# Optimization experiments

Measured on AMD Instinct MI355X. Metric: run time of the kernel, lower is better.

Reference implementation:

```python
import jax, jax.numpy as jnp
import numpy as np
import math

D_MODEL = 1024
NUM_HEADS = 16
HEAD_DIM = D_MODEL // NUM_HEADS


def _sinusoidal_pe(seq_len, dim, dtype=jnp.float32):
    # Matches RotaryPositionEmbedding buffer: pe[:,0::2]=sin, pe[:,1::2]=cos
    pos = jnp.arange(seq_len, dtype=jnp.float32)[:, None]            # [S,1]
    div = jnp.exp(jnp.arange(0, dim, 2, dtype=jnp.float32) * (-math.log(10000.0) / dim))  # [dim/2]
    ang = pos * div[None, :]                                          # [S,dim/2]
    pe = jnp.stack([jnp.sin(ang), jnp.cos(ang)], axis=-1).reshape(seq_len, dim)
    return pe.astype(dtype)


def setup_inputs() -> dict:
    key = jax.random.key(0)
    ks = jax.random.split(key, 11)
    B, S, D = 4, 1024, D_MODEL
    s = 1.0 / math.sqrt(D)
    inp = {
        "q": jax.random.normal(ks[0], (B, S, D), jnp.float32),
        "k": jax.random.normal(ks[1], (B, S, D), jnp.float32),
        "v": jax.random.normal(ks[2], (B, S, D), jnp.float32),
        "Wq": jax.random.normal(ks[3], (D, D), jnp.float32) * s,
        "bq": jax.random.normal(ks[4], (D,), jnp.float32) * s,
        "Wk": jax.random.normal(ks[5], (D, D), jnp.float32) * s,
        "bk": jax.random.normal(ks[6], (D,), jnp.float32) * s,
        "Wv": jax.random.normal(ks[7], (D, D), jnp.float32) * s,
        "bv": jax.random.normal(ks[8], (D,), jnp.float32) * s,
        "Wo": jax.random.normal(ks[9], (D, D), jnp.float32) * s,
        "bo": jax.random.normal(ks[10], (D,), jnp.float32) * s,
    }
    return inp


def reference(q, k, v, Wq, bq, Wk, bk, Wv, bv, Wo, bo):
    B, S, D = q.shape
    H, hd = NUM_HEADS, HEAD_DIM
    scale = hd ** -0.5

    def proj(x, W, b):  # nn.Linear: x @ W.T + b, then [B,H,S,hd]
        return (x @ W.T + b).reshape(B, S, H, hd).transpose(0, 2, 1, 3)

    qh = proj(q, Wq, bq)
    kh = proj(k, Wk, bk)
    vh = proj(v, Wv, bv)

    pe = _sinusoidal_pe(S, hd, qh.dtype)[None, None]  # [1,1,S,hd]
    qh = qh + pe
    kh = kh + pe

    scores = jnp.einsum("bhqd,bhkd->bhqk", qh, kh) * scale  # [B,H,S,S]
    attn = jax.nn.softmax(scores, axis=-1)
    out = jnp.einsum("bhqk,bhkd->bhqd", attn, vh)            # [B,H,S,hd]
    out = out.transpose(0, 2, 1, 3).reshape(B, S, D)
    return out @ Wo.T + bo
```

## Files before the change

kernel.cpp:

```cpp
#include <hip/hip_runtime.h>
#include <hip/hip_bf16.h>

#define B_  4
#define S_  1024
#define D_  1024
#define H_  16
#define HD_ 64

typedef __bf16 bf16;
typedef __bf16 bf16x8 __attribute__((ext_vector_type(8)));
typedef __bf16 bf16x4 __attribute__((ext_vector_type(4)));
typedef float  f32x4  __attribute__((ext_vector_type(4)));

__global__ __launch_bounds__(256)
void convert_all_kernel(const float* __restrict__ q, const float* __restrict__ k,
                        const float* __restrict__ v,
                        const float* __restrict__ Wq, const float* __restrict__ Wk,
                        const float* __restrict__ Wv, const float* __restrict__ Wo,
                        bf16* __restrict__ Xb, bf16* __restrict__ Wall)
{
    const size_t e = ((size_t)blockIdx.x * 256 + threadIdx.x) * 8;
    const size_t M4 = (size_t)1 << 22;
    const float* s;
    bf16* d;
    if (e < 3 * M4) {
        const int which = (int)(e >> 22);
        s = ((which == 0) ? q : (which == 1) ? k : v) + (e - ((size_t)which << 22));
        d = Xb + e;
    } else {
        const size_t r = e - 3 * M4;
        const int which = (int)(r >> 20);
        s = ((which == 0) ? Wq : (which == 1) ? Wk : (which == 2) ? Wv : Wo) +
            (r - ((size_t)which << 20));
        d = Wall + r;
    }
    const f32x4 a = *(const f32x4*)s;
    const f32x4 b = *(const f32x4*)(s + 4);
    bf16x8 o;
#pragma unroll
    for (int jj = 0; jj < 4; ++jj) { o[jj] = (bf16)a[jj]; o[jj + 4] = (bf16)b[jj]; }
    *(bf16x8*)d = o;
}

__global__ __launch_bounds__(256)
void qkv_proj_kernel(const bf16* __restrict__ Xb, const bf16* __restrict__ Wall,
                     const float* __restrict__ bq, const float* __restrict__ bk,
                     const float* __restrict__ bv,
                     bf16* __restrict__ Qh, bf16* __restrict__ Kh,
                     bf16* __restrict__ Vt)
{
    __shared__ __align__(16) bf16 sA[128 * 32];
    __shared__ __align__(16) bf16 sB[128 * 32];

    const int blk  = blockIdx.x;
    const int mIdx = blk & 31;
    const int t    = blk >> 5;
    const int nIdx = t & 7;
    const int z    = t >> 3;

    const int m0 = mIdx * 128, n0 = nIdx * 128;
    const bf16* __restrict__ X = Xb + ((size_t)z << 22);
    const bf16* __restrict__ W = Wall + ((size_t)z << 20);
    const float* __restrict__ bias = (z == 0) ? bq : (z == 1) ? bk : bv;

    const int tid  = threadIdx.x;
    const int lane = tid & 63;
    const int wave = tid >> 6;
    const int lr   = lane & 15;
    const int lg   = lane >> 4;
    const int mw   = (wave >> 1) * 64;
    const int nw   = (wave & 1) * 64;
    const int srow = tid >> 2;
    const int skg  = (tid & 3) * 8;

    f32x4 acc[4][4];
#pragma unroll
    for (int i = 0; i < 4; ++i)
#pragma unroll
        for (int j = 0; j < 4; ++j) acc[i][j] = (f32x4){0.f, 0.f, 0.f, 0.f};

    const bf16* Ab = X + (size_t)(m0 + srow) * D_ + skg;
    const bf16* Wb = W + (size_t)(n0 + srow) * D_ + skg;

    bf16x8 ra[2], rb[2];
#pragma unroll
    for (int p = 0; p < 2; ++p) {
        ra[p] = *(const bf16x8*)(Ab + (size_t)(p * 64) * D_);
        rb[p] = *(const bf16x8*)(Wb + (size_t)(p * 64) * D_);
    }

    for (int kt = 0; kt < 32; ++kt) {
        __syncthreads();
#pragma unroll
        for (int p = 0; p < 2; ++p) {
            *(bf16x8*)(sA + p * 2048 + tid * 8) = ra[p];
            *(bf16x8*)(sB + p * 2048 + tid * 8) = rb[p];
        }
        __syncthreads();

        if (kt < 31) {
            const int k1 = (kt + 1) * 32;
#pragma unroll
            for (int p = 0; p < 2; ++p) {
                ra[p] = *(const bf16x8*)(Ab + (size_t)(p * 64) * D_ + k1);
                rb[p] = *(const bf16x8*)(Wb + (size_t)(p * 64) * D_ + k1);
            }
        }

        bf16x8 af[4], bfr[4];
#pragma unroll
        for (int i = 0; i < 4; ++i)
            af[i] = *(const bf16x8*)(sA + (mw + 16 * i + lr) * 32 + lg * 8);
#pragma unroll
        for (int j = 0; j < 4; ++j)
            bfr[j] = *(const bf16x8*)(sB + (nw + 16 * j + lr) * 32 + lg * 8);
#pragma unroll
        for (int i = 0; i < 4; ++i)
#pragma unroll
            for (int j = 0; j < 4; ++j)
                acc[i][j] = __builtin_amdgcn_mfma_f32_16x16x32_bf16(af[i], bfr[j],
                                                                    acc[i][j], 0, 0, 0);
    }

    if (z < 2) {
        bf16* dst = (z == 0) ? Qh : Kh;
        const float sc = (z == 0) ? 0.125f : 1.0f;
#pragma unroll
        for (int i = 0; i < 4; ++i) {
#pragma unroll
            for (int j = 0; j < 4; ++j) {
                const int n = n0 + nw + 16 * j + lr;
                const int h = n >> 6, d = n & 63;
                const float bn = bias[n];
                const float dv_rev = 0.15915494309189535f *
                    exp2f(-(float)(d & ~1) * 0.20762050593046648f);
#pragma unroll
                for (int r = 0; r < 4; ++r) {
                    const int m = m0 + mw + 16 * i + lg * 4 + r;
                    const int b = m >> 10, s = m & 1023;
                    float rev = (float)s * dv_rev;
                    rev -= floorf(rev);
                    const float sv = __builtin_amdgcn_sinf(rev);
                    const float cv = __builtin_amdgcn_cosf(rev);
                    const float pe  = (d & 1) ? cv : sv;
                    const float val = (acc[i][j][r] + bn + pe) * sc;
                    dst[(size_t)((b * H_ + h) * S_ + s) * HD_ + d] = (bf16)val;
                }
            }
        }
    } else {
#pragma unroll
        for (int i = 0; i < 4; ++i) {
            const int mb = m0 + mw + 16 * i + lg * 4;
            const int b = mb >> 10, sb = mb & 1023;
#pragma unroll
            for (int j = 0; j < 4; ++j) {
                const int n = n0 + nw + 16 * j + lr;
                const int h = n >> 6, d = n & 63;
                const float bn = bias[n];
                bf16x4 pk;
#pragma unroll
                for (int r = 0; r < 4; ++r) pk[r] = (bf16)(acc[i][j][r] + bn);
                *(bf16x4*)(Vt + (size_t)((b * H_ + h) * HD_ + d) * S_ + sb) = pk;
            }
        }
    }
}

#define LDK 72
__global__ __launch_bounds__(256)
void attn_kernel(const bf16* __restrict__ Qh, const bf16* __restrict__ Kh,
                 const bf16* __restrict__ Vt, bf16* __restrict__ att)
{
    __shared__ __align__(16) bf16 sK[64 * LDK];
    __shared__ __align__(16) bf16 sV[64 * LDK];
    __shared__ __align__(16) bf16 sP[4 * 32 * LDK];

    const int tid  = threadIdx.x;
    const int lane = tid & 63;
    const int wave = tid >> 6;
    const int lr   = lane & 15;
    const int lg   = lane >> 4;
    const int bh   = blockIdx.x & 63;
    const int qt   = blockIdx.x >> 6;
    const int qw   = qt * 128 + wave * 32;

    const bf16* Qb = Qh + (size_t)bh * S_ * HD_;
    const bf16* Kb = Kh + (size_t)bh * S_ * HD_;
    const bf16* Vb = Vt + (size_t)bh * HD_ * S_;

    bf16x8 qa[2][2];
#pragma unroll
    for (int i = 0; i < 2; ++i)
#pragma unroll
        for (int ks = 0; ks < 2; ++ks)
            qa[i][ks] = *(const bf16x8*)(Qb + (size_t)(qw + 16 * i + lr) * HD_ +
                                         ks * 32 + lg * 8);

    f32x4 o[2][4];
    float lsum[2][4];
#pragma unroll
    for (int i = 0; i < 2; ++i) {
#pragma unroll
        for (int jd = 0; jd < 4; ++jd) o[i][jd] = (f32x4){0.f, 0.f, 0.f, 0.f};
#pragma unroll
        for (int r = 0; r < 4; ++r) lsum[i][r] = 0.f;
    }

    bf16* const pw   = sP + wave * 32 * LDK;
    const int  srow  = tid >> 3;
    const int  scol  = (tid & 7) * 8;

    bf16x8 kv[2], vv[2];
#pragma unroll
    for (int p = 0; p < 2; ++p) {
        kv[p] = *(const bf16x8*)(Kb + (size_t)(p * 32 + srow) * HD_ + scol);
        vv[p] = *(const bf16x8*)(Vb + (size_t)(p * 32 + srow) * S_ + scol);
    }

    for (int kc = 0; kc < 16; ++kc) {
        __syncthreads();
#pragma unroll
        for (int p = 0; p < 2; ++p) {
            *(bf16x8*)(sK + (p * 32 + srow) * LDK + scol) = kv[p];
            *(bf16x8*)(sV + (p * 32 + srow) * LDK + scol) = vv[p];
        }
        __syncthreads();

        if (kc < 15) {
            const int kn = (kc + 1) * 64;
#pragma unroll
            for (int p = 0; p < 2; ++p) {
                kv[p] = *(const bf16x8*)(Kb + (size_t)(kn + p * 32 + srow) * HD_ + scol);
                vv[p] = *(const bf16x8*)(Vb + (size_t)(p * 32 + srow) * S_ + kn + scol);
            }
        }

        bf16x8 kb[4][2];
#pragma unroll
        for (int jk = 0; jk < 4; ++jk)
#pragma unroll
            for (int ks = 0; ks < 2; ++ks)
                kb[jk][ks] = *(const bf16x8*)(sK + (16 * jk + lr) * LDK + ks * 32 + lg * 8);

#pragma unroll
        for (int i = 0; i < 2; ++i)
#pragma unroll
            for (int jk = 0; jk < 4; ++jk) {
                f32x4 s = (f32x4){0.f, 0.f, 0.f, 0.f};
                s = __builtin_amdgcn_mfma_f32_16x16x32_bf16(qa[i][0], kb[jk][0], s, 0, 0, 0);
                s = __builtin_amdgcn_mfma_f32_16x16x32_bf16(qa[i][1], kb[jk][1], s, 0, 0, 0);
#pragma unroll
                for (int r = 0; r < 4; ++r) {
                    const float pp = __expf(s[r]);
                    lsum[i][r] += pp;
                    pw[(16 * i + lg * 4 + r) * LDK + 16 * jk + lr] = (bf16)pp;
                }
            }
        asm volatile("s_waitcnt lgkmcnt(0)" ::: "memory");

#pragma unroll
        for (int ks = 0; ks < 2; ++ks) {
            bf16x8 pa[2];
#pragma unroll
            for (int i = 0; i < 2; ++i)
                pa[i] = *(const bf16x8*)(pw + (16 * i + lr) * LDK + ks * 32 + lg * 8);
#pragma unroll
            for (int jd = 0; jd < 4; ++jd) {
                const bf16x8 vb = *(const bf16x8*)(sV + (16 * jd + lr) * LDK +
                                                   ks * 32 + lg * 8);
#pragma unroll
                for (int i = 0; i < 2; ++i)
                    o[i][jd] = __builtin_amdgcn_mfma_f32_16x16x32_bf16(pa[i], vb,
                                                                       o[i][jd], 0, 0, 0);
            }
        }
    }

    const int b = bh >> 4, h = bh & 15;
#pragma unroll
    for (int i = 0; i < 2; ++i)
#pragma unroll
        for (int r = 0; r < 4; ++r) {
            float l = lsum[i][r];
#pragma unroll
            for (int off = 1; off < 16; off <<= 1)
                l += __shfl_xor(l, off, 64);
            const float inv = 1.f / l;
            const int s = qw + 16 * i + lg * 4 + r;
#pragma unroll
            for (int jd = 0; jd < 4; ++jd) {
                const int d = 16 * jd + lr;
                att[(size_t)(b * S_ + s) * D_ + h * HD_ + d] = (bf16)(o[i][jd][r] * inv);
            }
        }
}

__global__ __launch_bounds__(256)
void out_proj_kernel(const bf16* __restrict__ A, const bf16* __restrict__ Wob,
                     const float* __restrict__ bo, float* __restrict__ out)
{
    __shared__ __align__(16) bf16 sA[64 * 32];
    __shared__ __align__(16) bf16 sB[128 * 32];

    const int blk  = blockIdx.x;
    const int mIdx = blk & 63;
    const int nIdx = blk >> 6;
    const int m0 = mIdx * 64, n0 = nIdx * 128;

    const int tid  = threadIdx.x;
    const int lane = tid & 63;
    const int wave = tid >> 6;
    const int lr   = lane & 15;
    const int lg   = lane >> 4;
    const int mw   = (wave >> 1) * 32;
    const int nw   = (wave & 1) * 64;
    const int srow = tid >> 2;
    const int skg  = (tid & 3) * 8;

    f32x4 acc[2][4];
#pragma unroll
    for (int i = 0; i < 2; ++i)
#pragma unroll
        for (int j = 0; j < 4; ++j) acc[i][j] = (f32x4){0.f, 0.f, 0.f, 0.f};

    const bf16* Ab = A   + (size_t)(m0 + srow) * D_ + skg;
    const bf16* Wb = Wob + (size_t)(n0 + srow) * D_ + skg;

    bf16x8 aa, wb[2];
    aa = *(const bf16x8*)(Ab);
#pragma unroll
    for (int p = 0; p < 2; ++p)
        wb[p] = *(const bf16x8*)(Wb + (size_t)(p * 64) * D_);

    for (int kt = 0; kt < 32; ++kt) {
        __syncthreads();
        *(bf16x8*)(sA + tid * 8) = aa;
#pragma unroll
        for (int p = 0; p < 2; ++p)
            *(bf16x8*)(sB + p * 2048 + tid * 8) = wb[p];
        __syncthreads();

        if (kt < 31) {
            const int k1 = (kt + 1) * 32;
            aa = *(const bf16x8*)(Ab + k1);
#pragma unroll
            for (int p = 0; p < 2; ++p)
                wb[p] = *(const bf16x8*)(Wb + (size_t)(p * 64) * D_ + k1);
        }

        bf16x8 af[2], bfr[4];
#pragma unroll
        for (int i = 0; i < 2; ++i)
            af[i] = *(const bf16x8*)(sA + (mw + 16 * i + lr) * 32 + lg * 8);
#pragma unroll
        for (int j = 0; j < 4; ++j)
            bfr[j] = *(const bf16x8*)(sB + (nw + 16 * j + lr) * 32 + lg * 8);
#pragma unroll
        for (int i = 0; i < 2; ++i)
#pragma unroll
            for (int j = 0; j < 4; ++j)
                acc[i][j] = __builtin_amdgcn_mfma_f32_16x16x32_bf16(af[i], bfr[j],
                                                                    acc[i][j], 0, 0, 0);
    }

#pragma unroll
    for (int i = 0; i < 2; ++i)
#pragma unroll
        for (int j = 0; j < 4; ++j) {
            const int n = n0 + nw + 16 * j + lr;
            const float bn = bo[n];
#pragma unroll
            for (int r = 0; r < 4; ++r) {
                const int m = m0 + mw + 16 * i + lg * 4 + r;
                out[(size_t)m * D_ + n] = acc[i][j][r] + bn;
            }
        }
}

extern "C" void kernel_launch(void* const* d_in, const int* in_sizes, int n_in,
                              void* d_out, int out_size, void* d_ws, size_t ws_size,
                              hipStream_t stream)
{
    const float* q  = (const float*)d_in[0];
    const float* k  = (const float*)d_in[1];
    const float* v  = (const float*)d_in[2];
    const float* Wq = (const float*)d_in[3];
    const float* bq = (const float*)d_in[4];
    const float* Wk = (const float*)d_in[5];
    const float* bk = (const float*)d_in[6];
    const float* Wv = (const float*)d_in[7];
    const float* bv = (const float*)d_in[8];
    const float* Wo = (const float*)d_in[9];
    const float* bo = (const float*)d_in[10];

    char* ws = (char*)d_ws;
    const size_t MB8 = (size_t)8 * 1024 * 1024;
    bf16* Qh  = (bf16*)(ws);
    bf16* Kh  = (bf16*)(ws + MB8);
    bf16* Vt  = (bf16*)(ws + 2 * MB8);
    bf16* att = (bf16*)(ws + 3 * MB8);
    bf16* Xb   = (bf16*)(ws + 4 * MB8);
    bf16* Wall = (bf16*)(ws + 7 * MB8);

    convert_all_kernel<<<8192, 256, 0, stream>>>(q, k, v, Wq, Wk, Wv, Wo,
                                                 Xb, Wall);
    qkv_proj_kernel<<<768, 256, 0, stream>>>(Xb, Wall, bq, bk, bv, Qh, Kh, Vt);
    attn_kernel<<<512, 256, 0, stream>>>(Qh, Kh, Vt, att);
    out_proj_kernel<<<512, 256, 0, stream>>>(att, Wall + ((size_t)3 << 20),
                                             bo, (float*)d_out);
}
```

Before: 213.7 us.

## Fuse all four stages into one cooperative persistent kernel with grid syncs

Replaces the four separate launches (convert, QKV projection, attention, output projection) with one cooperative kernel of 768 blocks that runs each stage in turn and separates them with grid.sync. Stage bodies become inline device functions sharing one 36 KB shared-memory buffer. The aim is to remove launch gaps and tail effects between kernels. In exchange, every block reserves the largest shared-memory footprint, occupancy is capped by the launch bounds, 256 blocks sit idle during the attention and output stages, and each grid barrier has a cost. If the cooperative launch fails, it falls back to the original four launches.

```diff
diff --git a/kernel.cpp b/kernel.cpp
--- a/kernel.cpp
+++ b/kernel.cpp
@@ -1,5 +1,8 @@
 #include <hip/hip_runtime.h>
 #include <hip/hip_bf16.h>
+#include <hip/hip_cooperative_groups.h>
+
+namespace cg = cooperative_groups;
 
 #define B_  4
 #define S_  1024
@@ -12,14 +15,14 @@
 typedef __bf16 bf16x4 __attribute__((ext_vector_type(4)));
 typedef float  f32x4  __attribute__((ext_vector_type(4)));
 
-__global__ __launch_bounds__(256)
-void convert_all_kernel(const float* __restrict__ q, const float* __restrict__ k,
-                        const float* __restrict__ v,
-                        const float* __restrict__ Wq, const float* __restrict__ Wk,
-                        const float* __restrict__ Wv, const float* __restrict__ Wo,
-                        bf16* __restrict__ Xb, bf16* __restrict__ Wall)
-{
-    const size_t e = ((size_t)blockIdx.x * 256 + threadIdx.x) * 8;
+
+__device__ __forceinline__ void convert_body(
+    size_t u, const float* __restrict__ q, const float* __restrict__ k,
+    const float* __restrict__ v, const float* __restrict__ Wq,
+    const float* __restrict__ Wk, const float* __restrict__ Wv,
+    const float* __restrict__ Wo, bf16* __restrict__ Xb, bf16* __restrict__ Wall)
+{
+    const size_t e  = u * 8;
     const size_t M4 = (size_t)1 << 22;
     const float* s;
     bf16* d;
@@ -42,17 +45,15 @@
     *(bf16x8*)d = o;
 }
 
-__global__ __launch_bounds__(256)
-void qkv_proj_kernel(const bf16* __restrict__ Xb, const bf16* __restrict__ Wall,
-                     const float* __restrict__ bq, const float* __restrict__ bk,
-                     const float* __restrict__ bv,
-                     bf16* __restrict__ Qh, bf16* __restrict__ Kh,
-                     bf16* __restrict__ Vt)
-{
-    __shared__ __align__(16) bf16 sA[128 * 32];
-    __shared__ __align__(16) bf16 sB[128 * 32];
-
-    const int blk  = blockIdx.x;
+__device__ __forceinline__ void qkv_body(
+    char* smem, int blk, const bf16* __restrict__ Xb, const bf16* __restrict__ Wall,
+    const float* __restrict__ bq, const float* __restrict__ bk,
+    const float* __restrict__ bv,
+    bf16* __restrict__ Qh, bf16* __restrict__ Kh, bf16* __restrict__ Vt)
+{
+    bf16* sA = (bf16*)smem;
+    bf16* sB = (bf16*)(smem + 8192);
+
     const int mIdx = blk & 31;
     const int t    = blk >> 5;
     const int nIdx = t & 7;
@@ -168,21 +169,21 @@
 }
 
 #define LDK 72
-__global__ __launch_bounds__(256)
-void attn_kernel(const bf16* __restrict__ Qh, const bf16* __restrict__ Kh,
-                 const bf16* __restrict__ Vt, bf16* __restrict__ att)
-{
-    __shared__ __align__(16) bf16 sK[64 * LDK];
-    __shared__ __align__(16) bf16 sV[64 * LDK];
-    __shared__ __align__(16) bf16 sP[4 * 32 * LDK];
+__device__ __forceinline__ void attn_body(
+    char* smem, int blk, const bf16* __restrict__ Qh, const bf16* __restrict__ Kh,
+    const bf16* __restrict__ Vt, bf16* __restrict__ att)
+{
+    bf16* sK = (bf16*)smem;
+    bf16* sV = (bf16*)(smem + 9216);
+    bf16* sP = (bf16*)(smem + 18432);
 
     const int tid  = threadIdx.x;
     const int lane = tid & 63;
     const int wave = tid >> 6;
     const int lr   = lane & 15;
     const int lg   = lane >> 4;
-    const int bh   = blockIdx.x & 63;
-    const int qt   = blockIdx.x >> 6;
+    const int bh   = blk & 63;
+    const int qt   = blk >> 6;
     const int qw   = qt * 128 + wave * 32;
 
     const bf16* Qb = Qh + (size_t)bh * S_ * HD_;
@@ -296,14 +297,13 @@
         }
 }
 
-__global__ __launch_bounds__(256)
-void out_proj_kernel(const bf16* __restrict__ A, const bf16* __restrict__ Wob,
-                     const float* __restrict__ bo, float* __restrict__ out)
-{
-    __shared__ __align__(16) bf16 sA[64 * 32];
-    __shared__ __align__(16) bf16 sB[128 * 32];
-
-    const int blk  = blockIdx.x;
+__device__ __forceinline__ void out_body(
+    char* smem, int blk, const bf16* __restrict__ A, const bf16* __restrict__ Wob,
+    const float* __restrict__ bo, float* __restrict__ out)
+{
+    bf16* sA = (bf16*)smem;
+    bf16* sB = (bf16*)(smem + 4096);
+
     const int mIdx = blk & 63;
     const int nIdx = blk >> 6;
     const int m0 = mIdx * 64, n0 = nIdx * 128;
@@ -376,6 +376,81 @@
                 out[(size_t)m * D_ + n] = acc[i][j][r] + bn;
             }
         }
+}
+
+__global__ __launch_bounds__(256, 3)
+void fused_kernel(const float* __restrict__ q, const float* __restrict__ k,
+                  const float* __restrict__ v,
+                  const float* __restrict__ Wq, const float* __restrict__ Wk,
+                  const float* __restrict__ Wv, const float* __restrict__ Wo,
+                  const float* __restrict__ bq, const float* __restrict__ bk,
+                  const float* __restrict__ bv, const float* __restrict__ bo,
+                  bf16* __restrict__ Xb, bf16* __restrict__ Wall,
+                  bf16* __restrict__ Qh, bf16* __restrict__ Kh,
+                  bf16* __restrict__ Vt, bf16* __restrict__ att,
+                  float* __restrict__ out)
+{
+    __shared__ __align__(16) char smem[36864];
+    cg::grid_group grid = cg::this_grid();
+
+    {
+        const size_t total8 = (size_t)2 * 1024 * 1024;
+        for (size_t u = (size_t)blockIdx.x * 256 + threadIdx.x; u < total8;
+             u += (size_t)768 * 256)
+            convert_body(u, q, k, v, Wq, Wk, Wv, Wo, Xb, Wall);
+    }
+    __threadfence();
+    grid.sync();
+
+    qkv_body(smem, blockIdx.x, Xb, Wall, bq, bk, bv, Qh, Kh, Vt);
+    __threadfence();
+    grid.sync();
+
+    if (blockIdx.x < 512)
+        attn_body(smem, blockIdx.x, Qh, Kh, Vt, att);
+    __threadfence();
+    grid.sync();
+
+    if (blockIdx.x < 512)
+        out_body(smem, blockIdx.x, att, Wall + ((size_t)3 << 20), bo, out);
+}
+
+__global__ __launch_bounds__(256)
+void convert_all_kernel(const float* __restrict__ q, const float* __restrict__ k,
+                        const float* __restrict__ v,
+                        const float* __restrict__ Wq, const float* __restrict__ Wk,
+                        const float* __restrict__ Wv, const float* __restrict__ Wo,
+                        bf16* __restrict__ Xb, bf16* __restrict__ Wall)
+{
+    convert_body((size_t)blockIdx.x * 256 + threadIdx.x, q, k, v, Wq, Wk, Wv, Wo,
+                 Xb, Wall);
+}
+
+__global__ __launch_bounds__(256)
+void qkv_proj_kernel(const bf16* __restrict__ Xb, const bf16* __restrict__ Wall,
+                     const float* __restrict__ bq, const float* __restrict__ bk,
+                     const float* __restrict__ bv,
+                     bf16* __restrict__ Qh, bf16* __restrict__ Kh,
+                     bf16* __restrict__ Vt)
+{
+    __shared__ __align__(16) char smem[16384];
+    qkv_body(smem, blockIdx.x, Xb, Wall, bq, bk, bv, Qh, Kh, Vt);
+}
+
+__global__ __launch_bounds__(256)
+void attn_kernel(const bf16* __restrict__ Qh, const bf16* __restrict__ Kh,
+                 const bf16* __restrict__ Vt, bf16* __restrict__ att)
+{
+    __shared__ __align__(16) char smem[36864];
+    attn_body(smem, blockIdx.x, Qh, Kh, Vt, att);
+}
+
+__global__ __launch_bounds__(256)
+void out_proj_kernel(const bf16* __restrict__ A, const bf16* __restrict__ Wob,
+                     const float* __restrict__ bo, float* __restrict__ out)
+{
+    __shared__ __align__(16) char smem[12288];
+    out_body(smem, blockIdx.x, A, Wob, bo, out);
 }
 
 extern "C" void kernel_launch(void* const* d_in, const int* in_sizes, int n_in,
@@ -396,17 +471,29 @@
 
     char* ws = (char*)d_ws;
     const size_t MB8 = (size_t)8 * 1024 * 1024;
-    bf16* Qh  = (bf16*)(ws);
-    bf16* Kh  = (bf16*)(ws + MB8);
-    bf16* Vt  = (bf16*)(ws + 2 * MB8);
-    bf16* att = (bf16*)(ws + 3 * MB8);
+    bf16* Qh   = (bf16*)(ws);
+    bf16* Kh   = (bf16*)(ws + MB8);
+    bf16* Vt   = (bf16*)(ws + 2 * MB8);
+    bf16* att  = (bf16*)(ws + 3 * MB8);
     bf16* Xb   = (bf16*)(ws + 4 * MB8);
     bf16* Wall = (bf16*)(ws + 7 * MB8);
-
-    convert_all_kernel<<<8192, 256, 0, stream>>>(q, k, v, Wq, Wk, Wv, Wo,
-                                                 Xb, Wall);
-    qkv_proj_kernel<<<768, 256, 0, stream>>>(Xb, Wall, bq, bk, bv, Qh, Kh, Vt);
-    attn_kernel<<<512, 256, 0, stream>>>(Qh, Kh, Vt, att);
-    out_proj_kernel<<<512, 256, 0, stream>>>(att, Wall + ((size_t)3 << 20),
-                                             bo, (float*)d_out);
-}
+    float* outp = (float*)d_out;
+
+    void* args[] = {
+        (void*)&q, (void*)&k, (void*)&v, (void*)&Wq, (void*)&Wk, (void*)&Wv,
+        (void*)&Wo, (void*)&bq, (void*)&bk, (void*)&bv, (void*)&bo,
+        (void*)&Xb, (void*)&Wall, (void*)&Qh, (void*)&Kh, (void*)&Vt,
+        (void*)&att, (void*)&outp
+    };
+    hipError_t err = hipLaunchCooperativeKernel((const void*)fused_kernel,
+                                                dim3(768), dim3(256), args, 0,
+                                                stream);
+    if (err != hipSuccess) {
+        convert_all_kernel<<<8192, 256, 0, stream>>>(q, k, v, Wq, Wk, Wv, Wo,
+                                                     Xb, Wall);
+        qkv_proj_kernel<<<768, 256, 0, stream>>>(Xb, Wall, bq, bk, bv, Qh, Kh, Vt);
+        attn_kernel<<<512, 256, 0, stream>>>(Qh, Kh, Vt, att);
+        out_proj_kernel<<<512, 256, 0, stream>>>(att, Wall + ((size_t)3 << 20),
+                                                 bo, outp);
+    }
+}
```

After: 750.5 us. +251.2%, slower.
